# Kernel tuning notes

Hardware: AMD Instinct MI355X
Metric: run time of the kernel (lower is better)

The kernel has to match this reference:

```python
import jax, jax.numpy as jnp
import numpy as np
from jax import lax

# Topology constants (windowed DAG: compute node i, at global index N_IN+i,
# reads the FANIN immediately preceding global node values).
N_IN = 16      # number of input nodes
FANIN = 16     # connections per compute node
N_NODES = 512  # topologically ordered compute nodes (hidden + output)
N_OUT = 64     # last N_OUT nodes in node_order are outputs
BATCH = 32768
T = N_IN + N_NODES  # total node count


def setup_inputs() -> dict:
    key = jax.random.key(0)
    k1, k2, k3, k4 = jax.random.split(key, 4)
    x = jax.random.normal(k1, (BATCH, N_IN), dtype=jnp.float32)
    # weights scaled down so tanh is not fully saturated through 512 layers
    weights = jax.random.normal(k2, (N_NODES, FANIN), dtype=jnp.float32) * 0.25
    biases = jax.random.normal(k3, (N_NODES,), dtype=jnp.float32) * 0.1
    responses = 1.0 + 0.1 * jax.random.normal(k4, (N_NODES,), dtype=jnp.float32)
    # src indices for node i: global indices [i, i+FANIN) (== previous FANIN nodes,
    # since N_IN == FANIN). Shape [N_NODES, FANIN], int32, all in [0, T).
    src_idx = (jnp.arange(N_NODES, dtype=jnp.int32)[:, None]
               + jnp.arange(FANIN, dtype=jnp.int32)[None, :]
               + (N_IN - FANIN))
    return {"x": x, "weights": weights, "biases": biases,
            "responses": responses, "src_idx": src_idx}


def _forward(x, weights, biases, responses, src_idx):
    B = x.shape[0]
    # values buffer [B, T]: inputs first, then compute nodes in topo order
    values0 = jnp.zeros((B, T), dtype=x.dtype).at[:, :N_IN].set(x)

    def body(values, xs):
        i, idx_row, w, b, r = xs
        src_vals = jnp.take(values, idx_row, axis=1)        # [B, FANIN] gather
        agg = src_vals @ w                                   # [B] weighted sum
        out = jnp.tanh(agg + b) * r                          # activation
        values = lax.dynamic_update_slice(values, out[:, None], (0, N_IN + i))
        return values, None

    ii = jnp.arange(N_NODES, dtype=jnp.int32)
    values, _ = lax.scan(body, values0, (ii, src_idx, weights, biases, responses))
    return values[:, T - N_OUT:]  # [B, N_OUT]


def reference(x, weights, biases, responses, src_idx):
    return _forward(x, weights, biases, responses, src_idx)
```

## Files before the change

### kernel.cpp

```cpp
#include <hip/hip_runtime.h>


typedef float v4f __attribute__((ext_vector_type(4)));

constexpr int kNOut     = 64;
constexpr int kBatch    = 32768;
constexpr int kQStrideF = 80;
constexpr int kLdsFloats = (128 + 3) * kQStrideF;
constexpr float kScale  = 2.8853900817779268f;

#define QPERM(X, CTRL) __int_as_float(__builtin_amdgcn_update_dpp(            \
    __float_as_int(X), __float_as_int(X), (CTRL), 0xF, 0xF, false))

#define PREFQ(S) {                                                            \
    asm volatile(                                                             \
      "ds_read_b128 %0, %5 offset:0\n\t"                                      \
      "ds_read_b128 %1, %5 offset:64\n\t"                                     \
      "ds_read_b128 %2, %5 offset:128\n\t"                                    \
      "ds_read_b128 %3, %5 offset:192\n\t"                                    \
      "ds_read_b128 %4, %5 offset:256"                                        \
      : "=&v"(qw0[S]), "=&v"(qw1[S]), "=&v"(qw2[S]), "=&v"(qw3[S]),           \
        "=&v"(qb[S])                                                          \
      : "v"(a));                                                              \
    a += kQStrideF * 4; }

#define WAITQ(S)                                                              \
    asm volatile("s_waitcnt lgkmcnt(15)"                                      \
      : "+v"(qw0[S]), "+v"(qw1[S]), "+v"(qw2[S]), "+v"(qw3[S]), "+v"(qb[S]));

#define NODE1(QW, BSV, WA, WB, WC, WD) {                                      \
    float ini = is_l0 ? (BSV) : 0.0f;                                         \
    float p = fmaf((WA), (QW).x, ini);                                        \
    p = fmaf((WB), (QW).y, p);                                                \
    p = fmaf((WC), (QW).z, p);                                                \
    p = fmaf((WD), (QW).w, p);                                                \
    float s1 = p + QPERM(p, 0xB1);                   \
    float sf = s1 + QPERM(s1, 0x4E);                 \
    float ex = __builtin_amdgcn_exp2f(sf);                                    \
    float uu = __builtin_amdgcn_rcpf(ex + 1.0f);                              \
    float tn = fmaf(-2.0f, uu, 1.0f);             \
    float mg = QPERM((WA), 0x39);                    \
    (WA) = is_l3 ? tn : mg; }

#define NODEQ(S) {                                                            \
    PREFQ(((S) + 3) & 3)                                                      \
    WAITQ(S)                                                                  \
    v4f f0 = qw0[S], f1 = qw1[S], f2 = qw2[S], f3 = qw3[S], fb = qb[S];       \
    NODE1(f0, fb.x, r0, r1, r2, r3)                                           \
    NODE1(f1, fb.y, r1, r2, r3, r0)                                           \
    NODE1(f2, fb.z, r2, r3, r0, r1)                                           \
    NODE1(f3, fb.w, r3, r0, r1, r2) }

__global__ __launch_bounds__(512) void neat_fwd(
    const float* __restrict__ x,
    const float* __restrict__ w,
    const float* __restrict__ bias,
    const float* __restrict__ resp,
    float* __restrict__ out)
{
    __shared__ alignas(16) float ldsw[kLdsFloats];
    __shared__ float rst[512];

    const int t  = threadIdx.x;
    const int jl = t & 3;
    const bool is_l0 = (jl == 0);
    const bool is_l3 = (jl == 3);

    rst[t] = resp[t];
    __syncthreads();

    const float4* __restrict__ w4 = reinterpret_cast<const float4*>(w);
    #pragma unroll
    for (int k = 0; k < 4; ++k) {
        int i4 = t + k * 512;
        float4 v = w4[i4];
        int n = i4 >> 2, k4 = i4 & 3;
        int s0 = n + 4 * k4;
        float f0 = kScale * ((s0 + 0 < 16) ? 1.0f : rst[s0 - 16]);
        float f1 = kScale * ((s0 + 1 < 16) ? 1.0f : rst[s0 - 15]);
        float f2 = kScale * ((s0 + 2 < 16) ? 1.0f : rst[s0 - 14]);
        float f3 = kScale * ((s0 + 3 < 16) ? 1.0f : rst[s0 - 13]);
        float4 sc = make_float4(v.x * f0, v.y * f1, v.z * f2, v.w * f3);
        *reinterpret_cast<float4*>(
            &ldsw[(n >> 2) * kQStrideF + (n & 3) * 16 + k4 * 4]) = sc;
    }
    {
        float bs = bias[t] * kScale;
        int q = t >> 2, s = t & 3;
        #pragma unroll
        for (int rep = 0; rep < 4; ++rep)
            ldsw[q * kQStrideF + 64 + rep * 4 + s] = bs;
    }

    const int e = blockIdx.x * 128 + (t >> 2);
    const float4 xi = reinterpret_cast<const float4*>(x)[e * 4 + jl];
    float r0 = xi.x, r1 = xi.y, r2 = xi.z, r3 = xi.w;

    const float4* __restrict__ rr4 = reinterpret_cast<const float4*>(resp);
    const float4 rv0 = rr4[112 + jl], rv1 = rr4[116 + jl],
                 rv2 = rr4[120 + jl], rv3 = rr4[124 + jl];

    float* __restrict__ op = out + (size_t)e * kNOut + jl * 4;

    __syncthreads();

    unsigned int a = (unsigned int)(unsigned long long)(&ldsw[0])
                   + (unsigned int)(jl << 4);

    v4f qw0[4], qw1[4], qw2[4], qw3[4], qb[4];
    PREFQ(0) PREFQ(1) PREFQ(2)

    #pragma unroll 1
    for (int g = 0; g < 32; ++g) {
        NODEQ(0) NODEQ(1) NODEQ(2) NODEQ(3)
        if (g >= 28) {
            float4 rv = (g == 28) ? rv0 : (g == 29) ? rv1
                      : (g == 30) ? rv2 : rv3;
            *reinterpret_cast<float4*>(op + (g - 28) * 16) =
                make_float4(r0 * rv.x, r1 * rv.y, r2 * rv.z, r3 * rv.w);
        }
    }

    asm volatile("s_waitcnt lgkmcnt(0)" ::: "memory");
}

extern "C" void kernel_launch(void* const* d_in, const int* in_sizes, int n_in,
                              void* d_out, int out_size, void* d_ws, size_t ws_size,
                              hipStream_t stream) {
    const float* x    = (const float*)d_in[0];
    const float* w    = (const float*)d_in[1];
    const float* bias = (const float*)d_in[2];
    const float* resp = (const float*)d_in[3];
    float* out = (float*)d_out;
    dim3 block(512);
    dim3 grid((kBatch * 4) / 512);
    hipLaunchKernelGGL(neat_fwd, grid, block, 0, stream, x, w, bias, resp, out);
}
```

Measured before the change: 101.2 us.

## Reparametrize tanh state and take newest input off the quad reduction chain

Node state is now kept as u = (1 - tanh)/2, so the final fma that rebuilt tanh drops out of the per-node serial chain. Response, scale and bias are folded into precomputed weights and a per-lane bias share. The newest predecessor's contribution (u_prev * w15) is added after the DPP quad reduction instead of inside it, so the reduction over older values can overlap with the previous node's exp/rcp. This shortens the latency-bound dependency chain, in exchange for a small extra prologue pass (a sums array and one more barrier) and a slightly different floating-point rounding order.

```diff
diff --git a/kernel.cpp b/kernel.cpp
--- a/kernel.cpp
+++ b/kernel.cpp
@@ -28,19 +28,21 @@
     asm volatile("s_waitcnt lgkmcnt(15)"                                      \
       : "+v"(qw0[S]), "+v"(qw1[S]), "+v"(qw2[S]), "+v"(qw3[S]), "+v"(qb[S]));
 
-#define NODE1(QW, BSV, WA, WB, WC, WD) {                                      \
-    float ini = is_l0 ? (BSV) : 0.0f;                                         \
-    float p = fmaf((WA), (QW).x, ini);                                        \
+#define NODE1(QW, INIV, WA, WB, WC, WD) {                                     \
+    float wmask = is_l3 ? 0.0f : (QW).w;             \
+    float w15b  = QPERM((QW).w, 0xFF);             \
+    float p = fmaf((WA), (QW).x, (INIV));                                     \
     p = fmaf((WB), (QW).y, p);                                                \
     p = fmaf((WC), (QW).z, p);                                                \
-    p = fmaf((WD), (QW).w, p);                                                \
+    p = fmaf((WD), wmask, p);                                                 \
     float s1 = p + QPERM(p, 0xB1);                   \
     float sf = s1 + QPERM(s1, 0x4E);                 \
-    float ex = __builtin_amdgcn_exp2f(sf);                                    \
-    float uu = __builtin_amdgcn_rcpf(ex + 1.0f);                              \
-    float tn = fmaf(-2.0f, uu, 1.0f);             \
     float mg = QPERM((WA), 0x39);                    \
-    (WA) = is_l3 ? tn : mg; }
+    float acc = fmaf(u_prev, w15b, sf);                \
+    float ex  = __builtin_amdgcn_exp2f(acc);                                  \
+    float un  = __builtin_amdgcn_rcpf(ex + 1.0f);                             \
+    u_prev = un;                                                              \
+    (WA) = is_l3 ? un : mg; }
 
 #define NODEQ(S) {                                                            \
     PREFQ(((S) + 3) & 3)                                                      \
@@ -60,10 +62,10 @@
 {
     __shared__ alignas(16) float ldsw[kLdsFloats];
     __shared__ float rst[512];
+    __shared__ float sums[512];
 
     const int t  = threadIdx.x;
     const int jl = t & 3;
-    const bool is_l0 = (jl == 0);
     const bool is_l3 = (jl == 3);
 
     rst[t] = resp[t];
@@ -76,31 +78,45 @@
         float4 v = w4[i4];
         int n = i4 >> 2, k4 = i4 & 3;
         int s0 = n + 4 * k4;
-        float f0 = kScale * ((s0 + 0 < 16) ? 1.0f : rst[s0 - 16]);
-        float f1 = kScale * ((s0 + 1 < 16) ? 1.0f : rst[s0 - 15]);
-        float f2 = kScale * ((s0 + 2 < 16) ? 1.0f : rst[s0 - 14]);
-        float f3 = kScale * ((s0 + 3 < 16) ? 1.0f : rst[s0 - 13]);
-        float4 sc = make_float4(v.x * f0, v.y * f1, v.z * f2, v.w * f3);
+        float rho0 = (s0 + 0 < 16) ? 1.0f : rst[s0 - 16];
+        float rho1 = (s0 + 1 < 16) ? 1.0f : rst[s0 - 15];
+        float rho2 = (s0 + 2 < 16) ? 1.0f : rst[s0 - 14];
+        float rho3 = (s0 + 3 < 16) ? 1.0f : rst[s0 - 13];
+        float wr0 = v.x * rho0, wr1 = v.y * rho1,
+              wr2 = v.z * rho2, wr3 = v.w * rho3;
+        float ps = (wr0 + wr1) + (wr2 + wr3);
+        ps += QPERM(ps, 0xB1);
+        ps += QPERM(ps, 0x4E);
+        if (jl == 0) sums[n] = ps;
+        const float m2k = -2.0f * kScale;
+        float4 sc = make_float4(wr0 * m2k, wr1 * m2k, wr2 * m2k, wr3 * m2k);
         *reinterpret_cast<float4*>(
             &ldsw[(n >> 2) * kQStrideF + (n & 3) * 16 + k4 * 4]) = sc;
     }
+    __syncthreads();
+
     {
-        float bs = bias[t] * kScale;
+        float Bq = (bias[t] + sums[t]) * (kScale * 0.25f);
         int q = t >> 2, s = t & 3;
         #pragma unroll
         for (int rep = 0; rep < 4; ++rep)
-            ldsw[q * kQStrideF + 64 + rep * 4 + s] = bs;
+            ldsw[q * kQStrideF + 64 + rep * 4 + s] = Bq;
     }
 
     const int e = blockIdx.x * 128 + (t >> 2);
     const float4 xi = reinterpret_cast<const float4*>(x)[e * 4 + jl];
-    float r0 = xi.x, r1 = xi.y, r2 = xi.z, r3 = xi.w;
+    float r0 = fmaf(-0.5f, xi.x, 0.5f);
+    float r1 = fmaf(-0.5f, xi.y, 0.5f);
+    float r2 = fmaf(-0.5f, xi.z, 0.5f);
+    float r3 = fmaf(-0.5f, xi.w, 0.5f);
 
     const float4* __restrict__ rr4 = reinterpret_cast<const float4*>(resp);
     const float4 rv0 = rr4[112 + jl], rv1 = rr4[116 + jl],
                  rv2 = rr4[120 + jl], rv3 = rr4[124 + jl];
 
     float* __restrict__ op = out + (size_t)e * kNOut + jl * 4;
+
+    float u_prev = QPERM(r3, 0xFF);
 
     __syncthreads();
 
@@ -116,8 +132,12 @@
         if (g >= 28) {
             float4 rv = (g == 28) ? rv0 : (g == 29) ? rv1
                       : (g == 30) ? rv2 : rv3;
+            float t0 = fmaf(-2.0f, r0, 1.0f);
+            float t1 = fmaf(-2.0f, r1, 1.0f);
+            float t2 = fmaf(-2.0f, r2, 1.0f);
+            float t3 = fmaf(-2.0f, r3, 1.0f);
             *reinterpret_cast<float4*>(op + (g - 28) * 16) =
-                make_float4(r0 * rv.x, r1 * rv.y, r2 * rv.z, r3 * rv.w);
+                make_float4(t0 * rv.x, t1 * rv.y, t2 * rv.z, t3 * rv.w);
         }
     }
 
```

After: 103.0 us. About the same (+1.8%).

## Run one batch element per thread with scalar-loaded weights and sigmoid reparametrization

Applied to the files above, without the earlier changes.

Replaces the 4-lanes-per-element LDS/DPP scheme with one element per thread. Each thread keeps the 16-value sliding window in registers, and weights are read through scalar s_load_dwordx16 from a packed workspace buffer filled by a new prep kernel. The tanh is reparametrized as a sigmoid variable, with response and bias folded into the weights, so each node costs 16 FMAs plus exp and rcp, with no cross-lane permutes or selects. The trade-offs are an extra kernel launch, only 512 single-wave blocks, and scalar-load waits (lgkmcnt(0)) on every node pair.

```diff
diff --git a/kernel.cpp b/kernel.cpp
--- a/kernel.cpp
+++ b/kernel.cpp
@@ -1,123 +1,151 @@
 #include <hip/hip_runtime.h>
 
 
-typedef float v4f __attribute__((ext_vector_type(4)));
+typedef float sf16 __attribute__((ext_vector_type(16)));
+typedef float sf2  __attribute__((ext_vector_type(2)));
 
-constexpr int kNOut     = 64;
-constexpr int kBatch    = 32768;
-constexpr int kQStrideF = 80;
-constexpr int kLdsFloats = (128 + 3) * kQStrideF;
+constexpr int   kBatch  = 32768;
 constexpr float kScale  = 2.8853900817779268f;
+constexpr int   kSgF    = 272;
 
-#define QPERM(X, CTRL) __int_as_float(__builtin_amdgcn_update_dpp(            \
-    __float_as_int(X), __float_as_int(X), (CTRL), 0xF, 0xF, false))
+__global__ __launch_bounds__(64) void neat_prep(
+    const float* __restrict__ w, const float* __restrict__ bias,
+    const float* __restrict__ resp, float* __restrict__ pk)
+{
+    const int n = blockIdx.x * 64 + threadIdx.x;
+    const float4* w4 = reinterpret_cast<const float4*>(w) + n * 4;
+    float4 a0 = w4[0], a1 = w4[1], a2 = w4[2], a3 = w4[3];
+    const float m2k = -2.0f * kScale;
+    float sum = 0.0f;
+    float ws0,ws1,ws2,ws3,ws4,ws5,ws6,ws7,ws8,ws9,ws10,ws11,ws12,ws13,ws14,ws15;
+    #define DO(J, V) { float rho = (n + (J) < 16) ? 1.0f : resp[n + (J) - 16]; \
+                       float wr = (V) * rho; sum += wr; ws##J = wr * m2k; }
+    DO(0,a0.x) DO(1,a0.y) DO(2,a0.z)  DO(3,a0.w)
+    DO(4,a1.x) DO(5,a1.y) DO(6,a1.z)  DO(7,a1.w)
+    DO(8,a2.x) DO(9,a2.y) DO(10,a2.z) DO(11,a2.w)
+    DO(12,a3.x) DO(13,a3.y) DO(14,a3.z) DO(15,a3.w)
+    #undef DO
+    const float B = (bias[n] + sum) * kScale;
+    const int sg = n >> 4, j = n & 15;
+    float* gb = pk + sg * kSgF + j * 16;
+    reinterpret_cast<float4*>(gb)[0] = make_float4(ws0,  ws1,  ws2,  ws3);
+    reinterpret_cast<float4*>(gb)[1] = make_float4(ws4,  ws5,  ws6,  ws7);
+    reinterpret_cast<float4*>(gb)[2] = make_float4(ws8,  ws9,  ws10, ws11);
+    reinterpret_cast<float4*>(gb)[3] = make_float4(ws12, ws13, ws14, ws15);
+    pk[sg * kSgF + 256 + j] = B;
+}
 
-#define PREFQ(S) {                                                            \
-    asm volatile(                                                             \
-      "ds_read_b128 %0, %5 offset:0\n\t"                                      \
-      "ds_read_b128 %1, %5 offset:64\n\t"                                     \
-      "ds_read_b128 %2, %5 offset:128\n\t"                                    \
-      "ds_read_b128 %3, %5 offset:192\n\t"                                    \
-      "ds_read_b128 %4, %5 offset:256"                                        \
-      : "=&v"(qw0[S]), "=&v"(qw1[S]), "=&v"(qw2[S]), "=&v"(qw3[S]),           \
-        "=&v"(qb[S])                                                          \
-      : "v"(a));                                                              \
-    a += kQStrideF * 4; }
+#define SLOAD(S, BASEV, OFF)                                                  \
+    asm volatile("s_load_dwordx16 %0, %3, %4\n\t"                             \
+                 "s_load_dwordx16 %1, %3, %5\n\t"                             \
+                 "s_load_dwordx2  %2, %3, %6"                                 \
+      : "=s"(wA##S), "=s"(wB##S), "=s"(mm##S)                                 \
+      : "s"(BASEV), "n"(OFF), "n"((OFF) + 64), "n"(1024 + ((OFF) >> 4)));
 
-#define WAITQ(S)                                                              \
-    asm volatile("s_waitcnt lgkmcnt(15)"                                      \
-      : "+v"(qw0[S]), "+v"(qw1[S]), "+v"(qw2[S]), "+v"(qw3[S]), "+v"(qb[S]));
+#define SWAIT(S)                                                              \
+    asm volatile("s_waitcnt lgkmcnt(0)"                                       \
+      : "+s"(wA##S), "+s"(wB##S), "+s"(mm##S));
 
-#define NODE1(QW, BSV, WA, WB, WC, WD) {                                      \
-    float ini = is_l0 ? (BSV) : 0.0f;                                         \
-    float p = fmaf((WA), (QW).x, ini);                                        \
-    p = fmaf((WB), (QW).y, p);                                                \
-    p = fmaf((WC), (QW).z, p);                                                \
-    p = fmaf((WD), (QW).w, p);                                                \
-    float s1 = p + QPERM(p, 0xB1);                   \
-    float sf = s1 + QPERM(s1, 0x4E);                 \
-    float ex = __builtin_amdgcn_exp2f(sf);                                    \
-    float uu = __builtin_amdgcn_rcpf(ex + 1.0f);                              \
-    float tn = fmaf(-2.0f, uu, 1.0f);             \
-    float mg = QPERM((WA), 0x39);                    \
-    (WA) = is_l3 ? tn : mg; }
+#define NODE(W, BB, T0,T1,T2,T3,T4,T5,T6,T7,T8,T9,T10,T11,T12,T13,T14,T15, OUTR) { \
+    float p0 = fmaf((T0), (W)[0], (BB));                                      \
+    p0 = fmaf((T1), (W)[1], p0);                                              \
+    p0 = fmaf((T2), (W)[2], p0);                                              \
+    p0 = fmaf((T3), (W)[3], p0);                                              \
+    float p1 = (T4) * (W)[4];                                                 \
+    p1 = fmaf((T5), (W)[5], p1);                                              \
+    p1 = fmaf((T6), (W)[6], p1);                                              \
+    p1 = fmaf((T7), (W)[7], p1);                                              \
+    float p2 = (T8) * (W)[8];                                                 \
+    p2 = fmaf((T9),  (W)[9],  p2);                                            \
+    p2 = fmaf((T10), (W)[10], p2);                                            \
+    p2 = fmaf((T11), (W)[11], p2);                                            \
+    float p3 = (T12) * (W)[12];                                               \
+    p3 = fmaf((T13), (W)[13], p3);                                            \
+    p3 = fmaf((T14), (W)[14], p3);                                            \
+    p3 = fmaf((T15), (W)[15], p3);           \
+    float sz = (p0 + p1) + (p2 + p3);                                         \
+    float ez = __builtin_amdgcn_exp2f(sz);                                    \
+    (OUTR) = __builtin_amdgcn_rcpf(ez + 1.0f); }
 
-#define NODEQ(S) {                                                            \
-    PREFQ(((S) + 3) & 3)                                                      \
-    WAITQ(S)                                                                  \
-    v4f f0 = qw0[S], f1 = qw1[S], f2 = qw2[S], f3 = qw3[S], fb = qb[S];       \
-    NODE1(f0, fb.x, r0, r1, r2, r3)                                           \
-    NODE1(f1, fb.y, r1, r2, r3, r0)                                           \
-    NODE1(f2, fb.z, r2, r3, r0, r1)                                           \
-    NODE1(f3, fb.w, r3, r0, r1, r2) }
-
-__global__ __launch_bounds__(512) void neat_fwd(
+__global__ __launch_bounds__(64) void neat_fwd(
     const float* __restrict__ x,
-    const float* __restrict__ w,
-    const float* __restrict__ bias,
     const float* __restrict__ resp,
+    const float* __restrict__ pk,
     float* __restrict__ out)
 {
-    __shared__ alignas(16) float ldsw[kLdsFloats];
-    __shared__ float rst[512];
+    const int e = blockIdx.x * 64 + threadIdx.x;
 
-    const int t  = threadIdx.x;
-    const int jl = t & 3;
-    const bool is_l0 = (jl == 0);
-    const bool is_l3 = (jl == 3);
+    const float4* __restrict__ x4 = reinterpret_cast<const float4*>(x) + (size_t)e * 4;
+    float4 X0 = x4[0], X1 = x4[1], X2 = x4[2], X3 = x4[3];
+    float m0  = fmaf(-0.5f, X0.x, 0.5f), m1  = fmaf(-0.5f, X0.y, 0.5f);
+    float m2  = fmaf(-0.5f, X0.z, 0.5f), m3  = fmaf(-0.5f, X0.w, 0.5f);
+    float m4  = fmaf(-0.5f, X1.x, 0.5f), m5  = fmaf(-0.5f, X1.y, 0.5f);
+    float m6  = fmaf(-0.5f, X1.z, 0.5f), m7  = fmaf(-0.5f, X1.w, 0.5f);
+    float m8  = fmaf(-0.5f, X2.x, 0.5f), m9  = fmaf(-0.5f, X2.y, 0.5f);
+    float m10 = fmaf(-0.5f, X2.z, 0.5f), m11 = fmaf(-0.5f, X2.w, 0.5f);
+    float m12 = fmaf(-0.5f, X3.x, 0.5f), m13 = fmaf(-0.5f, X3.y, 0.5f);
+    float m14 = fmaf(-0.5f, X3.z, 0.5f), m15 = fmaf(-0.5f, X3.w, 0.5f);
 
-    rst[t] = resp[t];
-    __syncthreads();
+    float* __restrict__ op = out + (size_t)e * 64;
+    const uint64_t pkb = (uint64_t)pk;
 
-    const float4* __restrict__ w4 = reinterpret_cast<const float4*>(w);
-    #pragma unroll
-    for (int k = 0; k < 4; ++k) {
-        int i4 = t + k * 512;
-        float4 v = w4[i4];
-        int n = i4 >> 2, k4 = i4 & 3;
-        int s0 = n + 4 * k4;
-        float f0 = kScale * ((s0 + 0 < 16) ? 1.0f : rst[s0 - 16]);
-        float f1 = kScale * ((s0 + 1 < 16) ? 1.0f : rst[s0 - 15]);
-        float f2 = kScale * ((s0 + 2 < 16) ? 1.0f : rst[s0 - 14]);
-        float f3 = kScale * ((s0 + 3 < 16) ? 1.0f : rst[s0 - 13]);
-        float4 sc = make_float4(v.x * f0, v.y * f1, v.z * f2, v.w * f3);
-        *reinterpret_cast<float4*>(
-            &ldsw[(n >> 2) * kQStrideF + (n & 3) * 16 + k4 * 4]) = sc;
-    }
-    {
-        float bs = bias[t] * kScale;
-        int q = t >> 2, s = t & 3;
-        #pragma unroll
-        for (int rep = 0; rep < 4; ++rep)
-            ldsw[q * kQStrideF + 64 + rep * 4 + s] = bs;
-    }
+    sf16 wA0, wB0, wA1, wB1;
+    sf2  mm0, mm1;
 
-    const int e = blockIdx.x * 128 + (t >> 2);
-    const float4 xi = reinterpret_cast<const float4*>(x)[e * 4 + jl];
-    float r0 = xi.x, r1 = xi.y, r2 = xi.z, r3 = xi.w;
-
-    const float4* __restrict__ rr4 = reinterpret_cast<const float4*>(resp);
-    const float4 rv0 = rr4[112 + jl], rv1 = rr4[116 + jl],
-                 rv2 = rr4[120 + jl], rv3 = rr4[124 + jl];
-
-    float* __restrict__ op = out + (size_t)e * kNOut + jl * 4;
-
-    __syncthreads();
-
-    unsigned int a = (unsigned int)(unsigned long long)(&ldsw[0])
-                   + (unsigned int)(jl << 4);
-
-    v4f qw0[4], qw1[4], qw2[4], qw3[4], qb[4];
-    PREFQ(0) PREFQ(1) PREFQ(2)
+    SLOAD(0, pkb, 0)
 
     #pragma unroll 1
     for (int g = 0; g < 32; ++g) {
-        NODEQ(0) NODEQ(1) NODEQ(2) NODEQ(3)
+        const uint64_t base  = pkb + (uint64_t)g * 1088u;
+        const uint64_t base2 = base + 1088u;
+
+        SWAIT(0) SLOAD(1, base, 128)
+        NODE(wA0, mm0[0], m0,m1,m2,m3,m4,m5,m6,m7,m8,m9,m10,m11,m12,m13,m14,m15, m0)
+        NODE(wB0, mm0[1], m1,m2,m3,m4,m5,m6,m7,m8,m9,m10,m11,m12,m13,m14,m15,m0, m1)
+        SWAIT(1) SLOAD(0, base, 256)
+        NODE(wA1, mm1[0], m2,m3,m4,m5,m6,m7,m8,m9,m10,m11,m12,m13,m14,m15,m0,m1, m2)
+        NODE(wB1, mm1[1], m3,m4,m5,m6,m7,m8,m9,m10,m11,m12,m13,m14,m15,m0,m1,m2, m3)
+        SWAIT(0) SLOAD(1, base, 384)
+        NODE(wA0, mm0[0], m4,m5,m6,m7,m8,m9,m10,m11,m12,m13,m14,m15,m0,m1,m2,m3, m4)
+        NODE(wB0, mm0[1], m5,m6,m7,m8,m9,m10,m11,m12,m13,m14,m15,m0,m1,m2,m3,m4, m5)
+        SWAIT(1) SLOAD(0, base, 512)
+        NODE(wA1, mm1[0], m6,m7,m8,m9,m10,m11,m12,m13,m14,m15,m0,m1,m2,m3,m4,m5, m6)
+        NODE(wB1, mm1[1], m7,m8,m9,m10,m11,m12,m13,m14,m15,m0,m1,m2,m3,m4,m5,m6, m7)
+        SWAIT(0) SLOAD(1, base, 640)
+        NODE(wA0, mm0[0], m8,m9,m10,m11,m12,m13,m14,m15,m0,m1,m2,m3,m4,m5,m6,m7, m8)
+        NODE(wB0, mm0[1], m9,m10,m11,m12,m13,m14,m15,m0,m1,m2,m3,m4,m5,m6,m7,m8, m9)
+        SWAIT(1) SLOAD(0, base, 768)
+        NODE(wA1, mm1[0], m10,m11,m12,m13,m14,m15,m0,m1,m2,m3,m4,m5,m6,m7,m8,m9, m10)
+        NODE(wB1, mm1[1], m11,m12,m13,m14,m15,m0,m1,m2,m3,m4,m5,m6,m7,m8,m9,m10, m11)
+        SWAIT(0) SLOAD(1, base, 896)
+        NODE(wA0, mm0[0], m12,m13,m14,m15,m0,m1,m2,m3,m4,m5,m6,m7,m8,m9,m10,m11, m12)
+        NODE(wB0, mm0[1], m13,m14,m15,m0,m1,m2,m3,m4,m5,m6,m7,m8,m9,m10,m11,m12, m13)
+        SWAIT(1) SLOAD(0, base2, 0)
+        NODE(wA1, mm1[0], m14,m15,m0,m1,m2,m3,m4,m5,m6,m7,m8,m9,m10,m11,m12,m13, m14)
+        NODE(wB1, mm1[1], m15,m0,m1,m2,m3,m4,m5,m6,m7,m8,m9,m10,m11,m12,m13,m14, m15)
+
         if (g >= 28) {
-            float4 rv = (g == 28) ? rv0 : (g == 29) ? rv1
-                      : (g == 30) ? rv2 : rv3;
-            *reinterpret_cast<float4*>(op + (g - 28) * 16) =
-                make_float4(r0 * rv.x, r1 * rv.y, r2 * rv.z, r3 * rv.w);
+            const int mq = g - 28;
+            const float4* __restrict__ rr =
+                reinterpret_cast<const float4*>(resp + 448 + 16 * mq);
+            float4 R0 = rr[0], R1 = rr[1], R2 = rr[2], R3 = rr[3];
+            float4* o4 = reinterpret_cast<float4*>(op + 16 * mq);
+            o4[0] = make_float4(R0.x * fmaf(-2.0f, m0,  1.0f),
+                                R0.y * fmaf(-2.0f, m1,  1.0f),
+                                R0.z * fmaf(-2.0f, m2,  1.0f),
+                                R0.w * fmaf(-2.0f, m3,  1.0f));
+            o4[1] = make_float4(R1.x * fmaf(-2.0f, m4,  1.0f),
+                                R1.y * fmaf(-2.0f, m5,  1.0f),
+                                R1.z * fmaf(-2.0f, m6,  1.0f),
+                                R1.w * fmaf(-2.0f, m7,  1.0f));
+            o4[2] = make_float4(R2.x * fmaf(-2.0f, m8,  1.0f),
+                                R2.y * fmaf(-2.0f, m9,  1.0f),
+                                R2.z * fmaf(-2.0f, m10, 1.0f),
+                                R2.w * fmaf(-2.0f, m11, 1.0f));
+            o4[3] = make_float4(R3.x * fmaf(-2.0f, m12, 1.0f),
+                                R3.y * fmaf(-2.0f, m13, 1.0f),
+                                R3.z * fmaf(-2.0f, m14, 1.0f),
+                                R3.w * fmaf(-2.0f, m15, 1.0f));
         }
     }
 
@@ -132,7 +160,7 @@
     const float* bias = (const float*)d_in[2];
     const float* resp = (const float*)d_in[3];
     float* out = (float*)d_out;
-    dim3 block(512);
-    dim3 grid((kBatch * 4) / 512);
-    hipLaunchKernelGGL(neat_fwd, grid, block, 0, stream, x, w, bias, resp, out);
+    float* pk  = (float*)d_ws;
+    hipLaunchKernelGGL(neat_prep, dim3(8),   dim3(64), 0, stream, w, bias, resp, pk);
+    hipLaunchKernelGGL(neat_fwd,  dim3(512), dim3(64), 0, stream, x, resp, pk, out);
 }
```

Result: slower. 142.3 us (+40.6%).

## Carry sigmoid-domain state and store weights as fp16 with folded bias

Applied to the files above, without the earlier changes.

Node values are now held as u = 1/(1+e^{2x}), so tanh = 1-2u. That identity is folded into the weights (scaled by -2) and into a per-node bias (bias plus the weight sum), which removes one FMA per node on the serial chain. Weights are packed into fp16 pairs in LDS, which cuts LDS read traffic per 8-node region, and the prefetch pipeline is restructured to two buffers of 8 nodes. The trade-off is fp16 weight precision accumulating error across 512 dependent layers, plus per-element fp16-to-fp32 converts in the inner loop.

```diff
diff --git a/kernel.cpp b/kernel.cpp
--- a/kernel.cpp
+++ b/kernel.cpp
@@ -1,55 +1,68 @@
 #include <hip/hip_runtime.h>
 
 
-typedef float v4f __attribute__((ext_vector_type(4)));
+typedef float    v4f __attribute__((ext_vector_type(4)));
+typedef _Float16 h8  __attribute__((ext_vector_type(8)));
 
-constexpr int kNOut     = 64;
-constexpr int kBatch    = 32768;
-constexpr int kQStrideF = 80;
-constexpr int kLdsFloats = (128 + 3) * kQStrideF;
+constexpr int   kNOut   = 64;
+constexpr int   kBatch  = 32768;
+constexpr int   kSgF    = 96;
+constexpr int   kSgB    = 384;
+constexpr int   kLdsFloats = 65 * kSgF;
 constexpr float kScale  = 2.8853900817779268f;
 
 #define QPERM(X, CTRL) __int_as_float(__builtin_amdgcn_update_dpp(            \
     __float_as_int(X), __float_as_int(X), (CTRL), 0xF, 0xF, false))
 
-#define PREFQ(S) {                                                            \
+__device__ __forceinline__ unsigned pack2(float lo, float hi) {
+    _Float16 l = (_Float16)lo, h = (_Float16)hi;
+    unsigned short ul = __builtin_bit_cast(unsigned short, l);
+    unsigned short uh = __builtin_bit_cast(unsigned short, h);
+    return ((unsigned)uh << 16) | ul;
+}
+
+#define PREF(S) {                                                             \
     asm volatile(                                                             \
-      "ds_read_b128 %0, %5 offset:0\n\t"                                      \
-      "ds_read_b128 %1, %5 offset:64\n\t"                                     \
-      "ds_read_b128 %2, %5 offset:128\n\t"                                    \
-      "ds_read_b128 %3, %5 offset:192\n\t"                                    \
-      "ds_read_b128 %4, %5 offset:256"                                        \
+      "ds_read_b128 %0, %6 offset:0\n\t"                                      \
+      "ds_read_b128 %1, %6 offset:64\n\t"                                     \
+      "ds_read_b128 %2, %6 offset:128\n\t"                                    \
+      "ds_read_b128 %3, %6 offset:192\n\t"                                    \
+      "ds_read_b128 %4, %6 offset:256\n\t"                                    \
+      "ds_read_b128 %5, %6 offset:320"                                        \
       : "=&v"(qw0[S]), "=&v"(qw1[S]), "=&v"(qw2[S]), "=&v"(qw3[S]),           \
-        "=&v"(qb[S])                                                          \
+        "=&v"(qm0[S]), "=&v"(qm1[S])                                          \
       : "v"(a));                                                              \
-    a += kQStrideF * 4; }
+    a += kSgB; }
 
-#define WAITQ(S)                                                              \
-    asm volatile("s_waitcnt lgkmcnt(15)"                                      \
-      : "+v"(qw0[S]), "+v"(qw1[S]), "+v"(qw2[S]), "+v"(qw3[S]), "+v"(qb[S]));
+#define WAITR(S)                                                              \
+    asm volatile("s_waitcnt lgkmcnt(6)"                                       \
+      : "+v"(qw0[S]), "+v"(qw1[S]), "+v"(qw2[S]), "+v"(qw3[S]),               \
+        "+v"(qm0[S]), "+v"(qm1[S]));
 
-#define NODE1(QW, BSV, WA, WB, WC, WD) {                                      \
-    float ini = is_l0 ? (BSV) : 0.0f;                                         \
-    float p = fmaf((WA), (QW).x, ini);                                        \
-    p = fmaf((WB), (QW).y, p);                                                \
-    p = fmaf((WC), (QW).z, p);                                                \
-    p = fmaf((WD), (QW).w, p);                                                \
+#define NODE(WPAIR, H, BQ, A0,A1,A2,A3) {                                     \
+    h8 wh = __builtin_bit_cast(h8, (WPAIR));                                  \
+    float p = fmaf((A0), (float)wh[4*(H)+0], (BQ));                           \
+    p = fmaf((A1), (float)wh[4*(H)+1], p);                                    \
+    p = fmaf((A2), (float)wh[4*(H)+2], p);                                    \
+    p = fmaf((A3), (float)wh[4*(H)+3], p);                                    \
     float s1 = p + QPERM(p, 0xB1);                   \
-    float sf = s1 + QPERM(s1, 0x4E);                 \
-    float ex = __builtin_amdgcn_exp2f(sf);                                    \
-    float uu = __builtin_amdgcn_rcpf(ex + 1.0f);                              \
-    float tn = fmaf(-2.0f, uu, 1.0f);             \
-    float mg = QPERM((WA), 0x39);                    \
-    (WA) = is_l3 ? tn : mg; }
+    float s2 = s1 + QPERM(s1, 0x4E);                 \
+    float mg = QPERM((A0), 0x39);                    \
+    float ex = __builtin_amdgcn_exp2f(s2);                                    \
+    float un = __builtin_amdgcn_rcpf(ex + 1.0f);                              \
+    (A0) = is_l3 ? un : mg; }
 
-#define NODEQ(S) {                                                            \
-    PREFQ(((S) + 3) & 3)                                                      \
-    WAITQ(S)                                                                  \
-    v4f f0 = qw0[S], f1 = qw1[S], f2 = qw2[S], f3 = qw3[S], fb = qb[S];       \
-    NODE1(f0, fb.x, r0, r1, r2, r3)                                           \
-    NODE1(f1, fb.y, r1, r2, r3, r0)                                           \
-    NODE1(f2, fb.z, r2, r3, r0, r1)                                           \
-    NODE1(f3, fb.w, r3, r0, r1, r2) }
+#define REGION(SP, SC) {                                                      \
+    PREF(SP)                                                                  \
+    WAITR(SC)                                                                 \
+    NODE(qw0[SC], 0, qm0[SC].x, r0,r1,r2,r3)                                  \
+    NODE(qw0[SC], 1, qm0[SC].y, r1,r2,r3,r0)                                  \
+    NODE(qw1[SC], 0, qm0[SC].z, r2,r3,r0,r1)                                  \
+    NODE(qw1[SC], 1, qm0[SC].w, r3,r0,r1,r2)                                  \
+    NODE(qw2[SC], 0, qm1[SC].x, r0,r1,r2,r3)                                  \
+    NODE(qw2[SC], 1, qm1[SC].y, r1,r2,r3,r0)                                  \
+    NODE(qw3[SC], 0, qm1[SC].z, r2,r3,r0,r1)                                  \
+    NODE(qw3[SC], 1, qm1[SC].w, r3,r0,r1,r2) }
 
 __global__ __launch_bounds__(512) void neat_fwd(
     const float* __restrict__ x,
@@ -62,62 +75,72 @@
     __shared__ float rst[512];
 
     const int t  = threadIdx.x;
-    const int jl = t & 3;
-    const bool is_l0 = (jl == 0);
-    const bool is_l3 = (jl == 3);
+    const int jq = t & 3;
+    const bool is_l3 = (jq == 3);
 
     rst[t] = resp[t];
     __syncthreads();
 
-    const float4* __restrict__ w4 = reinterpret_cast<const float4*>(w);
-    #pragma unroll
-    for (int k = 0; k < 4; ++k) {
-        int i4 = t + k * 512;
-        float4 v = w4[i4];
-        int n = i4 >> 2, k4 = i4 & 3;
-        int s0 = n + 4 * k4;
-        float f0 = kScale * ((s0 + 0 < 16) ? 1.0f : rst[s0 - 16]);
-        float f1 = kScale * ((s0 + 1 < 16) ? 1.0f : rst[s0 - 15]);
-        float f2 = kScale * ((s0 + 2 < 16) ? 1.0f : rst[s0 - 14]);
-        float f3 = kScale * ((s0 + 3 < 16) ? 1.0f : rst[s0 - 13]);
-        float4 sc = make_float4(v.x * f0, v.y * f1, v.z * f2, v.w * f3);
-        *reinterpret_cast<float4*>(
-            &ldsw[(n >> 2) * kQStrideF + (n & 3) * 16 + k4 * 4]) = sc;
-    }
     {
-        float bs = bias[t] * kScale;
-        int q = t >> 2, s = t & 3;
-        #pragma unroll
-        for (int rep = 0; rep < 4; ++rep)
-            ldsw[q * kQStrideF + 64 + rep * 4 + s] = bs;
+        const int n = t;
+        const float4* wn = reinterpret_cast<const float4*>(w) + n * 4;
+        float4 a0 = wn[0], a1 = wn[1], a2 = wn[2], a3 = wn[3];
+        const float m2k = -2.0f * kScale;
+        float sum = 0.0f;
+        float ws0,ws1,ws2,ws3,ws4,ws5,ws6,ws7,ws8,ws9,ws10,ws11,ws12,ws13,ws14,ws15;
+        #define DO(J, V) { float rho = (n + (J) < 16) ? 1.0f : rst[n + (J) - 16]; \
+                           float wr = (V) * rho; sum += wr; ws##J = wr * m2k; }
+        DO(0,a0.x)  DO(1,a0.y)  DO(2,a0.z)  DO(3,a0.w)
+        DO(4,a1.x)  DO(5,a1.y)  DO(6,a1.z)  DO(7,a1.w)
+        DO(8,a2.x)  DO(9,a2.y)  DO(10,a2.z) DO(11,a2.w)
+        DO(12,a3.x) DO(13,a3.y) DO(14,a3.z) DO(15,a3.w)
+        #undef DO
+        const int sg = n >> 3, s = n & 7, m = s >> 1, h = s & 1;
+        unsigned* lu = reinterpret_cast<unsigned*>(ldsw);
+        int wi = sg * 96 + m * 16 + h * 2;
+        lu[wi + 0*4 + 0] = pack2(ws0,  ws1);   lu[wi + 0*4 + 1] = pack2(ws2,  ws3);
+        lu[wi + 1*4 + 0] = pack2(ws4,  ws5);   lu[wi + 1*4 + 1] = pack2(ws6,  ws7);
+        lu[wi + 2*4 + 0] = pack2(ws8,  ws9);   lu[wi + 2*4 + 1] = pack2(ws10, ws11);
+        lu[wi + 3*4 + 0] = pack2(ws12, ws13);  lu[wi + 3*4 + 1] = pack2(ws14, ws15);
+        float Bq = (bias[n] + sum) * (kScale * 0.25f);
+        const int c = s >> 2, p = s & 3;
+        int mi = sg * 96 + 64 + c * 16 + p;
+        ldsw[mi + 0]  = Bq;
+        ldsw[mi + 4]  = Bq;
+        ldsw[mi + 8]  = Bq;
+        ldsw[mi + 12] = Bq;
     }
 
     const int e = blockIdx.x * 128 + (t >> 2);
-    const float4 xi = reinterpret_cast<const float4*>(x)[e * 4 + jl];
-    float r0 = xi.x, r1 = xi.y, r2 = xi.z, r3 = xi.w;
+    const float4 xi = reinterpret_cast<const float4*>(x)[e * 4 + jq];
+    float r0 = fmaf(-0.5f, xi.x, 0.5f);
+    float r1 = fmaf(-0.5f, xi.y, 0.5f);
+    float r2 = fmaf(-0.5f, xi.z, 0.5f);
+    float r3 = fmaf(-0.5f, xi.w, 0.5f);
 
     const float4* __restrict__ rr4 = reinterpret_cast<const float4*>(resp);
-    const float4 rv0 = rr4[112 + jl], rv1 = rr4[116 + jl],
-                 rv2 = rr4[120 + jl], rv3 = rr4[124 + jl];
-
-    float* __restrict__ op = out + (size_t)e * kNOut + jl * 4;
+    float* __restrict__ op = out + (size_t)e * kNOut + jq * 4;
 
     __syncthreads();
 
     unsigned int a = (unsigned int)(unsigned long long)(&ldsw[0])
-                   + (unsigned int)(jl << 4);
+                   + (unsigned int)(jq << 4);
 
-    v4f qw0[4], qw1[4], qw2[4], qw3[4], qb[4];
-    PREFQ(0) PREFQ(1) PREFQ(2)
+    v4f qw0[2], qw1[2], qw2[2], qw3[2], qm0[2], qm1[2];
+    PREF(0)
 
     #pragma unroll 1
     for (int g = 0; g < 32; ++g) {
-        NODEQ(0) NODEQ(1) NODEQ(2) NODEQ(3)
+        REGION(1, 0)
+        REGION(0, 1)
         if (g >= 28) {
-            float4 rv = (g == 28) ? rv0 : (g == 29) ? rv1
-                      : (g == 30) ? rv2 : rv3;
-            *reinterpret_cast<float4*>(op + (g - 28) * 16) =
-                make_float4(r0 * rv.x, r1 * rv.y, r2 * rv.z, r3 * rv.w);
+            const int m_ = g - 28;
+            const float4 rv = rr4[112 + 4 * m_ + jq];
+            *reinterpret_cast<float4*>(op + 16 * m_) =
+                make_float4(fmaf(-2.0f, r0, 1.0f) * rv.x,
+                            fmaf(-2.0f, r1, 1.0f) * rv.y,
+                            fmaf(-2.0f, r2, 1.0f) * rv.z,
+                            fmaf(-2.0f, r3, 1.0f) * rv.w);
         }
     }
 
@@ -133,6 +156,6 @@
     const float* resp = (const float*)d_in[3];
     float* out = (float*)d_out;
     dim3 block(512);
-    dim3 grid((kBatch * 4) / 512);
+    dim3 grid(kBatch * 4 / 512);
     hipLaunchKernelGGL(neat_fwd, grid, block, 0, stream, x, w, bias, resp, out);
 }
```

Measured after the change: 97.44 us. 3.7% less time.
